# Kernel tuning notes

Measured on AMD Instinct MI355X. Metric: run time of the kernel, lower is better.

Reference implementation:

```python
import jax, jax.numpy as jnp
import numpy as np
from jax import lax

B, T, F, H = 128, 4096, 64, 128

def setup_inputs() -> dict:
    key = jax.random.key(0)
    k1, k2, k3, k4, k5 = jax.random.split(key, 5)
    s = 1.0 / np.sqrt(H)  # PyTorch LSTM init scale
    X = jax.random.normal(k1, (B, T, F), dtype=jnp.float32)
    W_ih = jax.random.uniform(k2, (4 * H, F), minval=-s, maxval=s, dtype=jnp.float32)
    W_hh = jax.random.uniform(k3, (4 * H, H), minval=-s, maxval=s, dtype=jnp.float32)
    b_ih = jax.random.uniform(k4, (4 * H,), minval=-s, maxval=s, dtype=jnp.float32)
    b_hh = jax.random.uniform(k5, (4 * H,), minval=-s, maxval=s, dtype=jnp.float32)
    return {"X": X, "W_ih": W_ih, "W_hh": W_hh, "b_ih": b_ih, "b_hh": b_hh}

def reference(X, W_ih, W_hh, b_ih, b_hh):
    # Faithful to the torch module: per-sequence LSTM with zero init state,
    # returning the output at the final timestep (== final hidden state).
    # PyTorch gate order: i, f, g, o.
    Bn, Tn, _ = X.shape
    Hn = W_hh.shape[1]
    # Precompute input contribution for all timesteps: [B, T, 4H]
    xg = jnp.einsum('btf,gf->btg', X, W_ih) + b_ih + b_hh
    xg_t = jnp.swapaxes(xg, 0, 1)  # [T, B, 4H]

    def step(carry, xg_step):
        h, c = carry
        gates = xg_step + h @ W_hh.T  # [B, 4H]
        i, f, g, o = jnp.split(gates, 4, axis=-1)
        i = jax.nn.sigmoid(i)
        f = jax.nn.sigmoid(f)
        g = jnp.tanh(g)
        o = jax.nn.sigmoid(o)
        c = f * c + i * g
        h = o * jnp.tanh(c)
        return (h, c), None

    h0 = jnp.zeros((Bn, Hn), dtype=X.dtype)
    c0 = jnp.zeros((Bn, Hn), dtype=X.dtype)
    (h_last, _), _ = lax.scan(step, (h0, c0), xg_t)
    return h_last  # [B, H]: the torch code's list of (1,1,H) outs, stacked
```

## Files before the change

### kernel.cpp

```cpp
#include <hip/hip_runtime.h>

#define B_  128
#define T_  4096
#define F_  64
#define H_  128
#define NT  512

typedef _Float16 half8_t __attribute__((ext_vector_type(8)));
typedef _Float16 half2_t __attribute__((ext_vector_type(2)));
typedef float    f32x4   __attribute__((ext_vector_type(4)));

__device__ __forceinline__ half2_t pack2(float a, float b) {
  half2_t r; r[0] = (_Float16)a; r[1] = (_Float16)b; return r;
}

__device__ __forceinline__ void wg_barrier() {
  __asm__ volatile("s_waitcnt lgkmcnt(0)\n\ts_barrier" ::: "memory");
}

__device__ __forceinline__ float fast_sigmoid(float x) {
  float e = __builtin_amdgcn_exp2f(x * -1.4426950408889634f);
  return __builtin_amdgcn_rcpf(1.0f + e);
}
__device__ __forceinline__ float fast_tanh(float x) {
  float e = __builtin_amdgcn_exp2f(x * -2.8853900817779268f);
  return 2.0f * __builtin_amdgcn_rcpf(1.0f + e) - 1.0f;
}

__global__ __launch_bounds__(NT, 2) void lstm_xg_kernel(
    const float* __restrict__ X,
    const float* __restrict__ Wih,
    const float* __restrict__ Whh,
    const float* __restrict__ bih,
    const float* __restrict__ bhh,
    float* __restrict__ out)
{
  const int tid  = threadIdx.x;
  const int b    = blockIdx.x;
  const int lane = tid & 63;
  const int w    = tid >> 6;
  const int lg   = lane >> 4;
  const int lc   = lane & 15;

  __shared__ __align__(16) _Float16 hbuf[2][H_];
  __shared__ __align__(16) _Float16 xst[2][16 * 72];
  __shared__ __align__(16) float    xg[2][16 * 512];

  half8_t Wf[4][6];
  f32x4   xinit[4];
#pragma unroll
  for (int g = 0; g < 4; ++g) {
    const int row = 128 * g + 16 * w + lc;
    const float bv = bih[row] + bhh[row];
    f32x4 bi = {bv, bv, bv, bv};
    xinit[g] = bi;
#pragma unroll
    for (int c = 0; c < 6; ++c) {
      const float* src = (c < 4) ? (Whh + (size_t)row * H_ + 32 * c + 8 * lg)
                                 : (Wih + (size_t)row * F_ + 32 * (c - 4) + 8 * lg);
      float4 lo = *(const float4*)(src);
      float4 hi = *(const float4*)(src + 4);
      half8_t v;
      v[0] = (_Float16)lo.x; v[1] = (_Float16)lo.y;
      v[2] = (_Float16)lo.z; v[3] = (_Float16)lo.w;
      v[4] = (_Float16)hi.x; v[5] = (_Float16)hi.y;
      v[6] = (_Float16)hi.z; v[7] = (_Float16)hi.w;
      Wf[g][c] = v;
    }
  }

  const float* xbase = X + (size_t)b * T_ * F_;
  const int    tp    = tid >> 5;
  const int    kp    = tid & 31;

  {
    float2 v0 = ((const float2*)xbase)[0 * 512 + tid];
    float2 v1 = ((const float2*)xbase)[1 * 512 + tid];
    *(half2_t*)&xst[0][tp * 72 + 2 * kp] = pack2(v0.x, v0.y);
    *(half2_t*)&xst[1][tp * 72 + 2 * kp] = pack2(v1.x, v1.y);
  }
  wg_barrier();

  const f32x4 zf = {0.0f, 0.0f, 0.0f, 0.0f};

  {
    half8_t a0 = *(const half8_t*)&xst[0][lc * 72 + 8 * lg];
    half8_t a1 = *(const half8_t*)&xst[0][lc * 72 + 32 + 8 * lg];
#pragma unroll
    for (int g = 0; g < 4; ++g) {
      f32x4 ab = __builtin_amdgcn_mfma_f32_16x16x32_f16(a0, Wf[g][4], xinit[g], 0, 0, 0);
      ab       = __builtin_amdgcn_mfma_f32_16x16x32_f16(a1, Wf[g][5], ab, 0, 0, 0);
      if (g == 0) { xinit[0] = xinit[0]; }
#pragma unroll
      for (int r = 0; r < 4; ++r)
        xg[0][(4 * lg + r) * 512 + (16 * w + lc) * 4 + g] = ab[r];
    }
  }
  wg_barrier();

  f32x4 pre[4], pB[4];
#pragma unroll
  for (int g = 0; g < 4; ++g) { pre[g] = zf; pB[g] = zf; }
  f32x4 xg4 = *(const f32x4*)&xg[0][0 * 512 + (16 * w + lc) * 4];

  float cs = 0.0f, hl = 0.0f;
  float2 xv = {0.0f, 0.0f};

#pragma unroll 2
  for (int t = 0; t < T_; ++t) {
    const int buf = t & 1;
    const int P   = t >> 4;
    const int tau = t & 15;

    float si = fast_sigmoid(pre[0][0] + pB[0][0] + xg4[0]);
    float sf = fast_sigmoid(pre[1][0] + pB[1][0] + xg4[1]);
    float sg = fast_tanh   (pre[2][0] + pB[2][0] + xg4[2]);
    float so = fast_sigmoid(pre[3][0] + pB[3][0] + xg4[3]);

    cs = sf * cs + si * sg;
    float hn = so * fast_tanh(cs);
    hl = hn;

    if (lane < 16) hbuf[buf][16 * w + lc] = (_Float16)hn;

    if (tau == 0) {
      const int sb = (P + 1) & 1;
      half8_t a0 = *(const half8_t*)&xst[sb][lc * 72 + 8 * lg];
      half8_t a1 = *(const half8_t*)&xst[sb][lc * 72 + 32 + 8 * lg];
#pragma unroll
      for (int g = 0; g < 4; ++g) {
        f32x4 ab = __builtin_amdgcn_mfma_f32_16x16x32_f16(a0, Wf[g][4], xinit[g], 0, 0, 0);
        ab       = __builtin_amdgcn_mfma_f32_16x16x32_f16(a1, Wf[g][5], ab, 0, 0, 0);
#pragma unroll
        for (int r = 0; r < 4; ++r)
          xg[sb][(4 * lg + r) * 512 + (16 * w + lc) * 4 + g] = ab[r];
      }
      int Pn = P + 2; if (Pn > (T_ / 16 - 1)) Pn = T_ / 16 - 1;
      xv = ((const float2*)xbase)[(size_t)Pn * 512 + tid];
    }
    if (tau == 8) {
      *(half2_t*)&xst[P & 1][tp * 72 + 2 * kp] = pack2(xv.x, xv.y);
    }

    wg_barrier();

    half8_t ah0 = *(const half8_t*)&hbuf[buf][ 0 + 8 * lg];
    half8_t ah1 = *(const half8_t*)&hbuf[buf][32 + 8 * lg];
    half8_t ah2 = *(const half8_t*)&hbuf[buf][64 + 8 * lg];
    half8_t ah3 = *(const half8_t*)&hbuf[buf][96 + 8 * lg];

    const int tn = t + 1;
    xg4 = *(const f32x4*)&xg[(tn >> 4) & 1][(tn & 15) * 512 + (16 * w + lc) * 4];

#pragma unroll
    for (int g = 0; g < 4; ++g) {
      f32x4 a  = __builtin_amdgcn_mfma_f32_16x16x32_f16(ah0, Wf[g][0], zf, 0, 0, 0);
      pre[g]   = __builtin_amdgcn_mfma_f32_16x16x32_f16(ah1, Wf[g][1], a, 0, 0, 0);
      f32x4 a2 = __builtin_amdgcn_mfma_f32_16x16x32_f16(ah2, Wf[g][2], zf, 0, 0, 0);
      pB[g]    = __builtin_amdgcn_mfma_f32_16x16x32_f16(ah3, Wf[g][3], a2, 0, 0, 0);
    }
  }

  if (lane < 16) out[(size_t)b * H_ + 16 * w + lc] = hl;
}

extern "C" void kernel_launch(void* const* d_in, const int* in_sizes, int n_in,
                              void* d_out, int out_size, void* d_ws, size_t ws_size,
                              hipStream_t stream) {
  const float* X   = (const float*)d_in[0];
  const float* Wih = (const float*)d_in[1];
  const float* Whh = (const float*)d_in[2];
  const float* bih = (const float*)d_in[3];
  const float* bhh = (const float*)d_in[4];
  float* out = (float*)d_out;

  lstm_xg_kernel<<<dim3(B_), dim3(NT), 0, stream>>>(X, Wih, Whh, bih, bhh, out);
}
```

Measured before the change: 1.954 ms.

## Halve workgroup to 4 waves with two hidden tiles per wave, prescale activations

Cuts the block from 512 to 256 threads, so each wave now owns two 16-row hidden tiles and issues twice as many MFMAs per step. The per-step s_barrier then only syncs 4 waves instead of 8. The activation scale factors (-log2e, -2log2e) are folded into the fp16 weights and biases, which removes a multiply per gate, and the xg shared buffer gets a padded stride. The cost is more registers per wave (Wf doubles), a longer serial MFMA chain per wave, and slightly different fp16 rounding because the weights are prescaled.

```diff
diff --git a/kernel.cpp b/kernel.cpp
--- a/kernel.cpp
+++ b/kernel.cpp
@@ -4,30 +4,35 @@
 #define T_  4096
 #define F_  64
 #define H_  128
-#define NT  512
+#define NT  256
+#define XGS 516
 
 typedef _Float16 half8_t __attribute__((ext_vector_type(8)));
-typedef _Float16 half2_t __attribute__((ext_vector_type(2)));
+typedef _Float16 half4_t __attribute__((ext_vector_type(4)));
 typedef float    f32x4   __attribute__((ext_vector_type(4)));
 
-__device__ __forceinline__ half2_t pack2(float a, float b) {
-  half2_t r; r[0] = (_Float16)a; r[1] = (_Float16)b; return r;
+#define LOG2E_NEG  (-1.4426950408889634f)
+#define LOG2E_NEG2 (-2.8853900817779268f)
+
+__device__ __forceinline__ half4_t pack4(float4 v) {
+  half4_t r;
+  r[0] = (_Float16)v.x; r[1] = (_Float16)v.y;
+  r[2] = (_Float16)v.z; r[3] = (_Float16)v.w;
+  return r;
 }
 
 __device__ __forceinline__ void wg_barrier() {
   __asm__ volatile("s_waitcnt lgkmcnt(0)\n\ts_barrier" ::: "memory");
 }
 
-__device__ __forceinline__ float fast_sigmoid(float x) {
-  float e = __builtin_amdgcn_exp2f(x * -1.4426950408889634f);
-  return __builtin_amdgcn_rcpf(1.0f + e);
-}
-__device__ __forceinline__ float fast_tanh(float x) {
-  float e = __builtin_amdgcn_exp2f(x * -2.8853900817779268f);
-  return 2.0f * __builtin_amdgcn_rcpf(1.0f + e) - 1.0f;
-}
-
-__global__ __launch_bounds__(NT, 2) void lstm_xg_kernel(
+__device__ __forceinline__ float sig_s(float xs) {
+  return __builtin_amdgcn_rcpf(1.0f + __builtin_amdgcn_exp2f(xs));
+}
+__device__ __forceinline__ float tanh_s(float ys) {
+  return 2.0f * __builtin_amdgcn_rcpf(1.0f + __builtin_amdgcn_exp2f(ys)) - 1.0f;
+}
+
+__global__ __launch_bounds__(NT, 1) void lstm_xg_kernel(
     const float* __restrict__ X,
     const float* __restrict__ Wih,
     const float* __restrict__ Whh,
@@ -44,40 +49,42 @@
 
   __shared__ __align__(16) _Float16 hbuf[2][H_];
   __shared__ __align__(16) _Float16 xst[2][16 * 72];
-  __shared__ __align__(16) float    xg[2][16 * 512];
-
-  half8_t Wf[4][6];
-  f32x4   xinit[4];
+  __shared__ __align__(16) float    xg[2][16 * XGS];
+
+  half8_t Wf[4][2][6];
+  float   bs[4][2];
 #pragma unroll
   for (int g = 0; g < 4; ++g) {
-    const int row = 128 * g + 16 * w + lc;
-    const float bv = bih[row] + bhh[row];
-    f32x4 bi = {bv, bv, bv, bv};
-    xinit[g] = bi;
-#pragma unroll
-    for (int c = 0; c < 6; ++c) {
-      const float* src = (c < 4) ? (Whh + (size_t)row * H_ + 32 * c + 8 * lg)
-                                 : (Wih + (size_t)row * F_ + 32 * (c - 4) + 8 * lg);
-      float4 lo = *(const float4*)(src);
-      float4 hi = *(const float4*)(src + 4);
-      half8_t v;
-      v[0] = (_Float16)lo.x; v[1] = (_Float16)lo.y;
-      v[2] = (_Float16)lo.z; v[3] = (_Float16)lo.w;
-      v[4] = (_Float16)hi.x; v[5] = (_Float16)hi.y;
-      v[6] = (_Float16)hi.z; v[7] = (_Float16)hi.w;
-      Wf[g][c] = v;
+    const float s = (g == 2) ? LOG2E_NEG2 : LOG2E_NEG;
+#pragma unroll
+    for (int u = 0; u < 2; ++u) {
+      const int row = 128 * g + 32 * w + 16 * u + lc;
+      bs[g][u] = (bih[row] + bhh[row]) * s;
+#pragma unroll
+      for (int c = 0; c < 6; ++c) {
+        const float* src = (c < 4) ? (Whh + (size_t)row * H_ + 32 * c + 8 * lg)
+                                   : (Wih + (size_t)row * F_ + 32 * (c - 4) + 8 * lg);
+        float4 lo = *(const float4*)(src);
+        float4 hi = *(const float4*)(src + 4);
+        half8_t v;
+        v[0] = (_Float16)(lo.x * s); v[1] = (_Float16)(lo.y * s);
+        v[2] = (_Float16)(lo.z * s); v[3] = (_Float16)(lo.w * s);
+        v[4] = (_Float16)(hi.x * s); v[5] = (_Float16)(hi.y * s);
+        v[6] = (_Float16)(hi.z * s); v[7] = (_Float16)(hi.w * s);
+        Wf[g][u][c] = v;
+      }
     }
   }
 
   const float* xbase = X + (size_t)b * T_ * F_;
-  const int    tp    = tid >> 5;
-  const int    kp    = tid & 31;
+  const int    tp    = tid >> 4;
+  const int    kp    = tid & 15;
 
   {
-    float2 v0 = ((const float2*)xbase)[0 * 512 + tid];
-    float2 v1 = ((const float2*)xbase)[1 * 512 + tid];
-    *(half2_t*)&xst[0][tp * 72 + 2 * kp] = pack2(v0.x, v0.y);
-    *(half2_t*)&xst[1][tp * 72 + 2 * kp] = pack2(v1.x, v1.y);
+    float4 v0 = ((const float4*)xbase)[0 * 256 + tid];
+    float4 v1 = ((const float4*)xbase)[1 * 256 + tid];
+    *(half4_t*)&xst[0][tp * 72 + 4 * kp] = pack4(v0);
+    *(half4_t*)&xst[1][tp * 72 + 4 * kp] = pack4(v1);
   }
   wg_barrier();
 
@@ -87,59 +94,80 @@
     half8_t a0 = *(const half8_t*)&xst[0][lc * 72 + 8 * lg];
     half8_t a1 = *(const half8_t*)&xst[0][lc * 72 + 32 + 8 * lg];
 #pragma unroll
-    for (int g = 0; g < 4; ++g) {
-      f32x4 ab = __builtin_amdgcn_mfma_f32_16x16x32_f16(a0, Wf[g][4], xinit[g], 0, 0, 0);
-      ab       = __builtin_amdgcn_mfma_f32_16x16x32_f16(a1, Wf[g][5], ab, 0, 0, 0);
-      if (g == 0) { xinit[0] = xinit[0]; }
-#pragma unroll
-      for (int r = 0; r < 4; ++r)
-        xg[0][(4 * lg + r) * 512 + (16 * w + lc) * 4 + g] = ab[r];
-    }
+    for (int g = 0; g < 4; ++g)
+#pragma unroll
+      for (int u = 0; u < 2; ++u) {
+        f32x4 bi = {bs[g][u], bs[g][u], bs[g][u], bs[g][u]};
+        f32x4 ab = __builtin_amdgcn_mfma_f32_16x16x32_f16(a0, Wf[g][u][4], bi, 0, 0, 0);
+        ab       = __builtin_amdgcn_mfma_f32_16x16x32_f16(a1, Wf[g][u][5], ab, 0, 0, 0);
+#pragma unroll
+        for (int r = 0; r < 4; ++r)
+          xg[0][(4 * lg + r) * XGS + (32 * w + 16 * u + lc) * 4 + g] = ab[r];
+      }
   }
   wg_barrier();
 
-  f32x4 pre[4], pB[4];
-#pragma unroll
-  for (int g = 0; g < 4; ++g) { pre[g] = zf; pB[g] = zf; }
-  f32x4 xg4 = *(const f32x4*)&xg[0][0 * 512 + (16 * w + lc) * 4];
-
-  float cs = 0.0f, hl = 0.0f;
-  float2 xv = {0.0f, 0.0f};
-
-#pragma unroll 2
+  f32x4 pre[4][2], pB[4][2];
+#pragma unroll
+  for (int g = 0; g < 4; ++g)
+#pragma unroll
+    for (int u = 0; u < 2; ++u) { pre[g][u] = zf; pB[g][u] = zf; }
+
+  f32x4 xg4a = *(const f32x4*)&xg[0][0 * XGS + (32 * w + lc) * 4];
+  f32x4 xg4b = *(const f32x4*)&xg[0][0 * XGS + (32 * w + 16 + lc) * 4];
+
+  float cs0 = 0.0f, cs1 = 0.0f, hl0 = 0.0f, hl1 = 0.0f;
+  float4 xv = {0.0f, 0.0f, 0.0f, 0.0f};
+
+#pragma unroll 16
   for (int t = 0; t < T_; ++t) {
     const int buf = t & 1;
     const int P   = t >> 4;
     const int tau = t & 15;
 
-    float si = fast_sigmoid(pre[0][0] + pB[0][0] + xg4[0]);
-    float sf = fast_sigmoid(pre[1][0] + pB[1][0] + xg4[1]);
-    float sg = fast_tanh   (pre[2][0] + pB[2][0] + xg4[2]);
-    float so = fast_sigmoid(pre[3][0] + pB[3][0] + xg4[3]);
-
-    cs = sf * cs + si * sg;
-    float hn = so * fast_tanh(cs);
-    hl = hn;
-
-    if (lane < 16) hbuf[buf][16 * w + lc] = (_Float16)hn;
+    float p00 = pre[0][0][0] + pB[0][0][0] + xg4a[0];
+    float p10 = pre[1][0][0] + pB[1][0][0] + xg4a[1];
+    float p20 = pre[2][0][0] + pB[2][0][0] + xg4a[2];
+    float p30 = pre[3][0][0] + pB[3][0][0] + xg4a[3];
+    float p01 = pre[0][1][0] + pB[0][1][0] + xg4b[0];
+    float p11 = pre[1][1][0] + pB[1][1][0] + xg4b[1];
+    float p21 = pre[2][1][0] + pB[2][1][0] + xg4b[2];
+    float p31 = pre[3][1][0] + pB[3][1][0] + xg4b[3];
+
+    float si0 = sig_s(p00), sf0 = sig_s(p10), sg0 = tanh_s(p20), so0 = sig_s(p30);
+    float si1 = sig_s(p01), sf1 = sig_s(p11), sg1 = tanh_s(p21), so1 = sig_s(p31);
+
+    cs0 = sf0 * cs0 + si0 * sg0;
+    cs1 = sf1 * cs1 + si1 * sg1;
+    float hn0 = so0 * tanh_s(cs0 * LOG2E_NEG2);
+    float hn1 = so1 * tanh_s(cs1 * LOG2E_NEG2);
+    hl0 = hn0; hl1 = hn1;
+
+    if (lane < 16) {
+      hbuf[buf][32 * w + lc]      = (_Float16)hn0;
+      hbuf[buf][32 * w + 16 + lc] = (_Float16)hn1;
+    }
 
     if (tau == 0) {
       const int sb = (P + 1) & 1;
       half8_t a0 = *(const half8_t*)&xst[sb][lc * 72 + 8 * lg];
       half8_t a1 = *(const half8_t*)&xst[sb][lc * 72 + 32 + 8 * lg];
 #pragma unroll
-      for (int g = 0; g < 4; ++g) {
-        f32x4 ab = __builtin_amdgcn_mfma_f32_16x16x32_f16(a0, Wf[g][4], xinit[g], 0, 0, 0);
-        ab       = __builtin_amdgcn_mfma_f32_16x16x32_f16(a1, Wf[g][5], ab, 0, 0, 0);
-#pragma unroll
-        for (int r = 0; r < 4; ++r)
-          xg[sb][(4 * lg + r) * 512 + (16 * w + lc) * 4 + g] = ab[r];
-      }
+      for (int g = 0; g < 4; ++g)
+#pragma unroll
+        for (int u = 0; u < 2; ++u) {
+          f32x4 bi = {bs[g][u], bs[g][u], bs[g][u], bs[g][u]};
+          f32x4 ab = __builtin_amdgcn_mfma_f32_16x16x32_f16(a0, Wf[g][u][4], bi, 0, 0, 0);
+          ab       = __builtin_amdgcn_mfma_f32_16x16x32_f16(a1, Wf[g][u][5], ab, 0, 0, 0);
+#pragma unroll
+          for (int r = 0; r < 4; ++r)
+            xg[sb][(4 * lg + r) * XGS + (32 * w + 16 * u + lc) * 4 + g] = ab[r];
+        }
       int Pn = P + 2; if (Pn > (T_ / 16 - 1)) Pn = T_ / 16 - 1;
-      xv = ((const float2*)xbase)[(size_t)Pn * 512 + tid];
+      xv = ((const float4*)xbase)[(size_t)Pn * 256 + tid];
     }
     if (tau == 8) {
-      *(half2_t*)&xst[P & 1][tp * 72 + 2 * kp] = pack2(xv.x, xv.y);
+      *(half4_t*)&xst[P & 1][tp * 72 + 4 * kp] = pack4(xv);
     }
 
     wg_barrier();
@@ -149,19 +177,27 @@
     half8_t ah2 = *(const half8_t*)&hbuf[buf][64 + 8 * lg];
     half8_t ah3 = *(const half8_t*)&hbuf[buf][96 + 8 * lg];
 
-    const int tn = t + 1;
-    xg4 = *(const f32x4*)&xg[(tn >> 4) & 1][(tn & 15) * 512 + (16 * w + lc) * 4];
-
-#pragma unroll
-    for (int g = 0; g < 4; ++g) {
-      f32x4 a  = __builtin_amdgcn_mfma_f32_16x16x32_f16(ah0, Wf[g][0], zf, 0, 0, 0);
-      pre[g]   = __builtin_amdgcn_mfma_f32_16x16x32_f16(ah1, Wf[g][1], a, 0, 0, 0);
-      f32x4 a2 = __builtin_amdgcn_mfma_f32_16x16x32_f16(ah2, Wf[g][2], zf, 0, 0, 0);
-      pB[g]    = __builtin_amdgcn_mfma_f32_16x16x32_f16(ah3, Wf[g][3], a2, 0, 0, 0);
-    }
-  }
-
-  if (lane < 16) out[(size_t)b * H_ + 16 * w + lc] = hl;
+    const int tn   = t + 1;
+    const int nb   = (tn >> 4) & 1;
+    const int ntau = tn & 15;
+    xg4a = *(const f32x4*)&xg[nb][ntau * XGS + (32 * w + lc) * 4];
+    xg4b = *(const f32x4*)&xg[nb][ntau * XGS + (32 * w + 16 + lc) * 4];
+
+#pragma unroll
+    for (int g = 0; g < 4; ++g)
+#pragma unroll
+      for (int u = 0; u < 2; ++u) {
+        f32x4 a   = __builtin_amdgcn_mfma_f32_16x16x32_f16(ah0, Wf[g][u][0], zf, 0, 0, 0);
+        pre[g][u] = __builtin_amdgcn_mfma_f32_16x16x32_f16(ah1, Wf[g][u][1], a, 0, 0, 0);
+        f32x4 a2  = __builtin_amdgcn_mfma_f32_16x16x32_f16(ah2, Wf[g][u][2], zf, 0, 0, 0);
+        pB[g][u]  = __builtin_amdgcn_mfma_f32_16x16x32_f16(ah3, Wf[g][u][3], a2, 0, 0, 0);
+      }
+  }
+
+  if (lane < 16) {
+    out[(size_t)b * H_ + 32 * w + lc]      = hl0;
+    out[(size_t)b * H_ + 32 * w + 16 + lc] = hl1;
+  }
 }
 
 extern "C" void kernel_launch(void* const* d_in, const int* in_sizes, int n_in,
```

Result: slower. 2.230 ms (+14.2%).

## Fold exp2 scaling into weights, pad xg stride, shorten per-step critical path

Applied to the files above, without the earlier changes.

The log2e scale factors used by sigmoid and tanh are pre-multiplied into the W_ih/W_hh fragments and biases. The cell state is also kept in scaled form, so each gate activation becomes a bare exp2 plus rcp with fused FMAs. The shared xg buffer row stride is padded from 512 to 516 floats to reduce LDS bank conflicts. The next-panel input-projection MFMAs and the X prefetch now run after the barrier, off the h-dependent critical path, and the time loop is unrolled 16x so the tau branches resolve at compile time. Risks are a little fp16 precision drift from scaling weights before the conversion, and higher register and code-size pressure from the deeper unroll.

```diff
diff --git a/kernel.cpp b/kernel.cpp
--- a/kernel.cpp
+++ b/kernel.cpp
@@ -5,10 +5,14 @@
 #define F_  64
 #define H_  128
 #define NT  512
+#define XGS 516
 
 typedef _Float16 half8_t __attribute__((ext_vector_type(8)));
 typedef _Float16 half2_t __attribute__((ext_vector_type(2)));
 typedef float    f32x4   __attribute__((ext_vector_type(4)));
+
+#define L2N1 (-1.4426950408889634f)
+#define L2N2 (-2.8853900817779268f)
 
 __device__ __forceinline__ half2_t pack2(float a, float b) {
   half2_t r; r[0] = (_Float16)a; r[1] = (_Float16)b; return r;
@@ -16,15 +20,6 @@
 
 __device__ __forceinline__ void wg_barrier() {
   __asm__ volatile("s_waitcnt lgkmcnt(0)\n\ts_barrier" ::: "memory");
-}
-
-__device__ __forceinline__ float fast_sigmoid(float x) {
-  float e = __builtin_amdgcn_exp2f(x * -1.4426950408889634f);
-  return __builtin_amdgcn_rcpf(1.0f + e);
-}
-__device__ __forceinline__ float fast_tanh(float x) {
-  float e = __builtin_amdgcn_exp2f(x * -2.8853900817779268f);
-  return 2.0f * __builtin_amdgcn_rcpf(1.0f + e) - 1.0f;
 }
 
 __global__ __launch_bounds__(NT, 2) void lstm_xg_kernel(
@@ -44,14 +39,15 @@
 
   __shared__ __align__(16) _Float16 hbuf[2][H_];
   __shared__ __align__(16) _Float16 xst[2][16 * 72];
-  __shared__ __align__(16) float    xg[2][16 * 512];
+  __shared__ __align__(16) float    xg[2][16 * XGS];
 
   half8_t Wf[4][6];
   f32x4   xinit[4];
 #pragma unroll
   for (int g = 0; g < 4; ++g) {
+    const float s = (g == 2) ? L2N2 : L2N1;
     const int row = 128 * g + 16 * w + lc;
-    const float bv = bih[row] + bhh[row];
+    const float bv = (bih[row] + bhh[row]) * s;
     f32x4 bi = {bv, bv, bv, bv};
     xinit[g] = bi;
 #pragma unroll
@@ -61,10 +57,10 @@
       float4 lo = *(const float4*)(src);
       float4 hi = *(const float4*)(src + 4);
       half8_t v;
-      v[0] = (_Float16)lo.x; v[1] = (_Float16)lo.y;
-      v[2] = (_Float16)lo.z; v[3] = (_Float16)lo.w;
-      v[4] = (_Float16)hi.x; v[5] = (_Float16)hi.y;
-      v[6] = (_Float16)hi.z; v[7] = (_Float16)hi.w;
+      v[0] = (_Float16)(lo.x * s); v[1] = (_Float16)(lo.y * s);
+      v[2] = (_Float16)(lo.z * s); v[3] = (_Float16)(lo.w * s);
+      v[4] = (_Float16)(hi.x * s); v[5] = (_Float16)(hi.y * s);
+      v[6] = (_Float16)(hi.z * s); v[7] = (_Float16)(hi.w * s);
       Wf[g][c] = v;
     }
   }
@@ -90,10 +86,9 @@
     for (int g = 0; g < 4; ++g) {
       f32x4 ab = __builtin_amdgcn_mfma_f32_16x16x32_f16(a0, Wf[g][4], xinit[g], 0, 0, 0);
       ab       = __builtin_amdgcn_mfma_f32_16x16x32_f16(a1, Wf[g][5], ab, 0, 0, 0);
-      if (g == 0) { xinit[0] = xinit[0]; }
 #pragma unroll
       for (int r = 0; r < 4; ++r)
-        xg[0][(4 * lg + r) * 512 + (16 * w + lc) * 4 + g] = ab[r];
+        xg[0][(4 * lg + r) * XGS + (16 * w + lc) * 4 + g] = ab[r];
     }
   }
   wg_barrier();
@@ -101,27 +96,46 @@
   f32x4 pre[4], pB[4];
 #pragma unroll
   for (int g = 0; g < 4; ++g) { pre[g] = zf; pB[g] = zf; }
-  f32x4 xg4 = *(const f32x4*)&xg[0][0 * 512 + (16 * w + lc) * 4];
+  f32x4 xg4 = *(const f32x4*)&xg[0][0 * XGS + (16 * w + lc) * 4];
 
-  float cs = 0.0f, hl = 0.0f;
+  float csS = 0.0f, hl = 0.0f;
   float2 xv = {0.0f, 0.0f};
 
-#pragma unroll 2
+#pragma unroll 16
   for (int t = 0; t < T_; ++t) {
     const int buf = t & 1;
     const int P   = t >> 4;
     const int tau = t & 15;
 
-    float si = fast_sigmoid(pre[0][0] + pB[0][0] + xg4[0]);
-    float sf = fast_sigmoid(pre[1][0] + pB[1][0] + xg4[1]);
-    float sg = fast_tanh   (pre[2][0] + pB[2][0] + xg4[2]);
-    float so = fast_sigmoid(pre[3][0] + pB[3][0] + xg4[3]);
+    float p0 = pre[0][0] + pB[0][0] + xg4[0];
+    float p1 = pre[1][0] + pB[1][0] + xg4[1];
+    float p2 = pre[2][0] + pB[2][0] + xg4[2];
+    float p3 = pre[3][0] + pB[3][0] + xg4[3];
 
-    cs = sf * cs + si * sg;
-    float hn = so * fast_tanh(cs);
+    float si = __builtin_amdgcn_rcpf(1.0f + __builtin_amdgcn_exp2f(p0));
+    float sf = __builtin_amdgcn_rcpf(1.0f + __builtin_amdgcn_exp2f(p1));
+    float rg = __builtin_amdgcn_rcpf(1.0f + __builtin_amdgcn_exp2f(p2));
+    float so = __builtin_amdgcn_rcpf(1.0f + __builtin_amdgcn_exp2f(p3));
+
+    float ai = si * L2N2;
+    csS = fmaf(sf, csS, fmaf(ai + ai, rg, -ai));
+
+    float so2 = so + so, son = -so;
+    float rh  = __builtin_amdgcn_rcpf(1.0f + __builtin_amdgcn_exp2f(csS));
+    float hn  = fmaf(so2, rh, son);
     hl = hn;
 
     if (lane < 16) hbuf[buf][16 * w + lc] = (_Float16)hn;
+
+    wg_barrier();
+
+    half8_t ah0 = *(const half8_t*)&hbuf[buf][ 0 + 8 * lg];
+    half8_t ah1 = *(const half8_t*)&hbuf[buf][32 + 8 * lg];
+    half8_t ah2 = *(const half8_t*)&hbuf[buf][64 + 8 * lg];
+    half8_t ah3 = *(const half8_t*)&hbuf[buf][96 + 8 * lg];
+
+    const int tn = t + 1;
+    xg4 = *(const f32x4*)&xg[(tn >> 4) & 1][(tn & 15) * XGS + (16 * w + lc) * 4];
 
     if (tau == 0) {
       const int sb = (P + 1) & 1;
@@ -133,7 +147,7 @@
         ab       = __builtin_amdgcn_mfma_f32_16x16x32_f16(a1, Wf[g][5], ab, 0, 0, 0);
 #pragma unroll
         for (int r = 0; r < 4; ++r)
-          xg[sb][(4 * lg + r) * 512 + (16 * w + lc) * 4 + g] = ab[r];
+          xg[sb][(4 * lg + r) * XGS + (16 * w + lc) * 4 + g] = ab[r];
       }
       int Pn = P + 2; if (Pn > (T_ / 16 - 1)) Pn = T_ / 16 - 1;
       xv = ((const float2*)xbase)[(size_t)Pn * 512 + tid];
@@ -141,16 +155,6 @@
     if (tau == 8) {
       *(half2_t*)&xst[P & 1][tp * 72 + 2 * kp] = pack2(xv.x, xv.y);
     }
-
-    wg_barrier();
-
-    half8_t ah0 = *(const half8_t*)&hbuf[buf][ 0 + 8 * lg];
-    half8_t ah1 = *(const half8_t*)&hbuf[buf][32 + 8 * lg];
-    half8_t ah2 = *(const half8_t*)&hbuf[buf][64 + 8 * lg];
-    half8_t ah3 = *(const half8_t*)&hbuf[buf][96 + 8 * lg];
-
-    const int tn = t + 1;
-    xg4 = *(const f32x4*)&xg[(tn >> 4) & 1][(tn & 15) * 512 + (16 * w + lc) * 4];
 
 #pragma unroll
     for (int g = 0; g < 4; ++g) {
```

After: 1.860 ms. -4.8%, faster.
